# Performance work log

Hardware: AMD Instinct MI355X
Metric: run time of the kernel (lower is better)

Reference implementation:

```python
import jax, jax.numpy as jnp
import numpy as np

N_NODES = 100000
D_IN = 128
D_OUT = 128
B, T, S = 8, 4096, 25


def setup_inputs() -> dict:
    key = jax.random.key(0)
    k1, k2, k3 = jax.random.split(key, 3)
    features = jax.random.normal(k1, (N_NODES, D_IN), dtype=jnp.float32)
    sample_res = jax.random.randint(k2, (B, T, S), 0, N_NODES, dtype=jnp.int64)
    # glorot-uniform init for [D_IN, D_OUT]
    limit = np.sqrt(6.0 / (D_IN + D_OUT)).astype(np.float32)
    weights = jax.random.uniform(k3, (D_IN, D_OUT), dtype=jnp.float32,
                                 minval=-limit, maxval=limit)
    return {"features": features, "sample_res": sample_res, "weights": weights}


def reference(features, sample_res, weights):
    # gather neighbor embeddings: [B, T, S, D]
    sampled = features[sample_res]
    # mean over sampled-neighbor axis -> [B, T, D]
    neigh_vecs = jnp.mean(sampled, axis=2)
    # shared linear transform + relu (bias=False per init defaults)
    out = jnp.einsum('btd,do->bto', neigh_vecs, weights)
    return jax.nn.relu(out)
```

## Files before the change

kernel.cpp:

```cpp
#include <hip/hip_runtime.h>


#define DEG 25
#define DIM 128
#define NPP 25000
#define NPP1 25001

typedef __attribute__((ext_vector_type(8))) short short8;
typedef __attribute__((ext_vector_type(4))) float floatx4;
typedef __attribute__((ext_vector_type(4))) unsigned int uintx4;

__device__ __forceinline__ unsigned short f2bf(float f) {
    unsigned u = __float_as_uint(f);
    return (unsigned short)((u + 0x7fffu + ((u >> 16) & 1u)) >> 16);
}

#define BSTRIDE 136

__global__ __launch_bounds__(256, 2) void gemm_fw(
    const float* __restrict__ A,
    const float* __restrict__ B,
    unsigned short* __restrict__ G,
    int M)
{
    __shared__ unsigned short sBt[DIM * BSTRIDE];

    const int tid = threadIdx.x;

    {
        const float4* B4 = (const float4*)B;
#pragma unroll
        for (int i = 0; i < 16; ++i) {
            const int linear = i * 256 + tid;
            const int k  = linear >> 5;
            const int c4 = linear & 31;
            const float4 v = B4[linear];
            const int n = c4 * 4;
            sBt[(n + 0) * BSTRIDE + k] = f2bf(v.x);
            sBt[(n + 1) * BSTRIDE + k] = f2bf(v.y);
            sBt[(n + 2) * BSTRIDE + k] = f2bf(v.z);
            sBt[(n + 3) * BSTRIDE + k] = f2bf(v.w);
        }
    }
    __syncthreads();

    const int wave = tid >> 6;
    const int lane = tid & 63;
    const int quad = lane >> 4;
    const int l16  = lane & 15;

    const int rw0 = blockIdx.x * 128 + wave * 32;

    floatx4 acc[2][8];
#pragma unroll
    for (int mt = 0; mt < 2; ++mt)
#pragma unroll
        for (int nt = 0; nt < 8; ++nt)
            acc[mt][nt] = (floatx4){0.f, 0.f, 0.f, 0.f};

#pragma unroll
    for (int kt = 0; kt < 4; ++kt) {
        const int k0 = kt * 32;

        short8 afrag[2];
#pragma unroll
        for (int mt = 0; mt < 2; ++mt) {
            int row = rw0 + mt * 16 + l16;
            if (row >= M) row = M - 1;
            const float* ap = A + (size_t)row * DIM + k0 + quad * 8;
            const float4 x = *(const float4*)ap;
            const float4 y = *(const float4*)(ap + 4);
            unsigned p0 = (unsigned)f2bf(x.x) | ((unsigned)f2bf(x.y) << 16);
            unsigned p1 = (unsigned)f2bf(x.z) | ((unsigned)f2bf(x.w) << 16);
            unsigned p2 = (unsigned)f2bf(y.x) | ((unsigned)f2bf(y.y) << 16);
            unsigned p3 = (unsigned)f2bf(y.z) | ((unsigned)f2bf(y.w) << 16);
            uintx4 packed = (uintx4){p0, p1, p2, p3};
            afrag[mt] = __builtin_bit_cast(short8, packed);
        }

#pragma unroll
        for (int nt = 0; nt < 8; ++nt) {
            const uintx4 u = *(const uintx4*)&sBt[(nt * 16 + l16) * BSTRIDE + k0 + quad * 8];
            const short8 bfrag = __builtin_bit_cast(short8, u);
#pragma unroll
            for (int mt = 0; mt < 2; ++mt)
                acc[mt][nt] = __builtin_amdgcn_mfma_f32_16x16x32_bf16(
                    afrag[mt], bfrag, acc[mt][nt], 0, 0, 0);
        }
    }

    __syncthreads();
    {
        unsigned short* sT = sBt + wave * (32 * BSTRIDE);
#pragma unroll
        for (int mt = 0; mt < 2; ++mt)
#pragma unroll
            for (int nt = 0; nt < 8; ++nt)
#pragma unroll
                for (int r = 0; r < 4; ++r)
                    sT[(mt * 16 + quad * 4 + r) * BSTRIDE + nt * 16 + l16] =
                        f2bf(acc[mt][nt][r]);
    }
    __syncthreads();
    {
        const unsigned short* sT = sBt + wave * (32 * BSTRIDE);
        const int oct   = lane & 7;
        const int nrow8 = lane >> 3;
        uintx4* G4 = (uintx4*)G;
#pragma unroll
        for (int g = 0; g < 4; ++g) {
            const int lrow = g * 8 + nrow8;
            const int node = rw0 + lrow;
            if (node < M) {
                const unsigned p     = (unsigned)node / NPP;
                const unsigned local = (unsigned)node - p * NPP;
#pragma unroll
                for (int h = 0; h < 2; ++h) {
                    const uintx4 u = *(const uintx4*)
                        &sT[lrow * BSTRIDE + h * 64 + oct * 8];
                    __builtin_nontemporal_store(u,
                        &G4[((size_t)(p * 2 + h) * NPP1 + local) * 8 + oct]);
                }
            }
        }
        if (blockIdx.x == 0 && tid < 64) {
            const int sl = tid >> 3, o = tid & 7;
            __builtin_nontemporal_store((uintx4){0, 0, 0, 0},
                &G4[((size_t)sl * NPP1 + NPP) * 8 + o]);
        }
    }
}

#define GRB 64

__global__ __launch_bounds__(256, 4) void gather_phased(
    const unsigned short* __restrict__ G,
    const int* __restrict__ idx,
    float* __restrict__ out,
    int n_rows)
{
    __shared__ int sRaw[GRB * DEG];
    __shared__ int sC[GRB][4][25];
    __shared__ int sCnt[GRB][4];

    const int tid  = threadIdx.x;
    const int h    = blockIdx.x & 1;
    const int rb   = blockIdx.x >> 1;
    const int row0 = rb * GRB;

    const int* ib = idx + (size_t)row0 * DEG;
    for (int i = tid; i < GRB * DEG; i += 256)
        sRaw[i] = __builtin_nontemporal_load(ib + i);
    __syncthreads();

    {
        const int row = tid >> 2;
        const int rg  = tid & 3;
        const int lo  = rg * NPP;
        int* dst = &sC[row][rg][0];
        int cnt = 0;
#pragma unroll
        for (int s = 0; s < DEG; ++s) {
            const unsigned d = (unsigned)(sRaw[row * DEG + s] - lo);
            if (d < NPP) dst[cnt++] = (int)d;
        }
        const int m = ((cnt + 4) / 5) * 5;
        for (int i = cnt; i < m; ++i) dst[i] = NPP;
        sCnt[row][rg] = m;
    }
    __syncthreads();

    const int oct   = tid & 7;
    const int rslot = tid >> 3;

    float acc[2][8];
#pragma unroll
    for (int rr = 0; rr < 2; ++rr)
#pragma unroll
        for (int j = 0; j < 8; ++j) acc[rr][j] = 0.f;

    for (int p = 0; p < 4; ++p) {
        const uintx4* __restrict__ Gc =
            (const uintx4*)G + (size_t)(p * 2 + h) * NPP1 * 8 + oct;
#pragma unroll
        for (int rr = 0; rr < 2; ++rr) {
            const int r = rslot + rr * 32;
            const int m = sCnt[r][p];
            const int* lp = &sC[r][p][0];
            for (int i = 0; i < m; i += 5) {
                const uintx4 v0 = Gc[(size_t)lp[i + 0] * 8];
                const uintx4 v1 = Gc[(size_t)lp[i + 1] * 8];
                const uintx4 v2 = Gc[(size_t)lp[i + 2] * 8];
                const uintx4 v3 = Gc[(size_t)lp[i + 3] * 8];
                const uintx4 v4 = Gc[(size_t)lp[i + 4] * 8];
#pragma unroll
                for (int k = 0; k < 5; ++k) {
                    const uintx4 v = (k == 0) ? v0 : (k == 1) ? v1 :
                                     (k == 2) ? v2 : (k == 3) ? v3 : v4;
                    acc[rr][0] += __uint_as_float(v.x << 16);
                    acc[rr][1] += __uint_as_float(v.x & 0xffff0000u);
                    acc[rr][2] += __uint_as_float(v.y << 16);
                    acc[rr][3] += __uint_as_float(v.y & 0xffff0000u);
                    acc[rr][4] += __uint_as_float(v.z << 16);
                    acc[rr][5] += __uint_as_float(v.z & 0xffff0000u);
                    acc[rr][6] += __uint_as_float(v.w << 16);
                    acc[rr][7] += __uint_as_float(v.w & 0xffff0000u);
                }
            }
        }
    }

    const float inv = 1.0f / 25.0f;
#pragma unroll
    for (int rr = 0; rr < 2; ++rr) {
        const int r = rslot + rr * 32;
        floatx4* op = (floatx4*)(out + (size_t)(row0 + r) * DIM + h * 64 + oct * 8);
        const floatx4 o0 = {fmaxf(acc[rr][0] * inv, 0.f), fmaxf(acc[rr][1] * inv, 0.f),
                            fmaxf(acc[rr][2] * inv, 0.f), fmaxf(acc[rr][3] * inv, 0.f)};
        const floatx4 o1 = {fmaxf(acc[rr][4] * inv, 0.f), fmaxf(acc[rr][5] * inv, 0.f),
                            fmaxf(acc[rr][6] * inv, 0.f), fmaxf(acc[rr][7] * inv, 0.f)};
        __builtin_nontemporal_store(o0, op);
        __builtin_nontemporal_store(o1, op + 1);
    }
}

#define RPB 16
#define CG 32

__device__ __forceinline__ float4 relu4(float4 v) {
    return make_float4(fmaxf(v.x, 0.f), fmaxf(v.y, 0.f),
                       fmaxf(v.z, 0.f), fmaxf(v.w, 0.f));
}

__global__ __launch_bounds__(256, 4) void gcn_fused(
    const float* __restrict__ F, const int* __restrict__ idx,
    const float* __restrict__ W, float* __restrict__ out, int n_rows)
{
    __shared__ float4 sV[RPB * CG];
    __shared__ int    sIdx[RPB * DEG];

    const float4* F4 = (const float4*)F;
    const float4* W4 = (const float4*)W;
    float4* out4 = (float4*)out;

    const int tid = threadIdx.x;
    const int row0 = blockIdx.x * RPB;

    for (int i = tid; i < RPB * DEG; i += 256)
        sIdx[i] = idx[(size_t)row0 * DEG + i];
    __syncthreads();

    const int cg = tid & 31;
    const int rs = tid >> 5;

#pragma unroll
    for (int rr = 0; rr < 2; ++rr) {
        const int r = rs + rr * 8;
        int j[DEG];
#pragma unroll
        for (int s = 0; s < DEG; ++s) j[s] = sIdx[r * DEG + s];
        float4 acc = make_float4(0.f, 0.f, 0.f, 0.f);
#pragma unroll
        for (int s = 0; s < DEG; ++s) {
            float4 f = F4[(size_t)j[s] * CG + cg];
            acc.x += f.x; acc.y += f.y; acc.z += f.z; acc.w += f.w;
        }
        const float inv = 1.0f / 25.0f;
        acc.x *= inv; acc.y *= inv; acc.z *= inv; acc.w *= inv;
        sV[r * CG + cg] = acc;
    }
    __syncthreads();

    const float4* vA = &sV[rs * CG];
    const float4* vB = &sV[(rs + 8) * CG];
    float4 o0 = make_float4(0.f, 0.f, 0.f, 0.f);
    float4 o1 = make_float4(0.f, 0.f, 0.f, 0.f);
#pragma unroll 4
    for (int d4 = 0; d4 < CG; ++d4) {
        const float4 a = vA[d4];
        const float4 b = vB[d4];
        const float4 w0 = W4[(size_t)(4 * d4 + 0) * CG + cg];
        const float4 w1 = W4[(size_t)(4 * d4 + 1) * CG + cg];
        const float4 w2 = W4[(size_t)(4 * d4 + 2) * CG + cg];
        const float4 w3 = W4[(size_t)(4 * d4 + 3) * CG + cg];
        o0.x += a.x*w0.x + a.y*w1.x + a.z*w2.x + a.w*w3.x;
        o0.y += a.x*w0.y + a.y*w1.y + a.z*w2.y + a.w*w3.y;
        o0.z += a.x*w0.z + a.y*w1.z + a.z*w2.z + a.w*w3.z;
        o0.w += a.x*w0.w + a.y*w1.w + a.z*w2.w + a.w*w3.w;
        o1.x += b.x*w0.x + b.y*w1.x + b.z*w2.x + b.w*w3.x;
        o1.y += b.x*w0.y + b.y*w1.y + b.z*w2.y + b.w*w3.y;
        o1.z += b.x*w0.z + b.y*w1.z + b.z*w2.z + b.w*w3.z;
        o1.w += b.x*w0.w + b.y*w1.w + b.z*w2.w + b.w*w3.w;
    }
    out4[(size_t)(row0 + rs) * CG + cg]     = relu4(o0);
    out4[(size_t)(row0 + rs + 8) * CG + cg] = relu4(o1);
}

extern "C" void kernel_launch(void* const* d_in, const int* in_sizes, int n_in,
                              void* d_out, int out_size, void* d_ws, size_t ws_size,
                              hipStream_t stream) {
    const float* F   = (const float*)d_in[0];
    const int*   idx = (const int*)d_in[1];
    const float* W   = (const float*)d_in[2];
    float* out = (float*)d_out;

    const int n_nodes = in_sizes[0] / DIM;
    const int n_rows  = in_sizes[1] / DEG;

    const size_t need = (size_t)8 * NPP1 * 64 * sizeof(unsigned short);

    if (n_nodes == 100000 && ws_size >= need && (n_rows & (GRB - 1)) == 0) {
        unsigned short* G = (unsigned short*)d_ws;
        gemm_fw<<<(n_nodes + 127) / 128, 256, 0, stream>>>(F, W, G, n_nodes);
        gather_phased<<<(n_rows / GRB) * 2, 256, 0, stream>>>(G, idx, out, n_rows);
    } else {
        gcn_fused<<<n_rows / RPB, 256, 0, stream>>>(F, idx, W, out, n_rows);
    }
}
```

Before: 128.6 us.

## Halve gather block rows, use ushort index lists, software-pipeline neighbor loads

The phased gather kernel now handles 32 rows per block with one row per 8-thread group instead of two, and targets 6 blocks per SM instead of 4. Compacted neighbor indices are stored as 16-bit values padded to multiples of 4, shrinking shared memory. The inner loop is software-pipelined: the next four bf16 rows are loaded before the current four are accumulated. The aim is more waves in flight and more overlapped memory latency on this random-gather-bound kernel. The cost is more blocks, more redundant index staging, and at least 4 padding loads per partition even when it has no neighbors.

```diff
diff --git a/kernel.cpp b/kernel.cpp
--- a/kernel.cpp
+++ b/kernel.cpp
@@ -131,16 +131,16 @@
     }
 }
 
-#define GRB 64
-
-__global__ __launch_bounds__(256, 4) void gather_phased(
+#define GRB 32
+
+__global__ __launch_bounds__(256, 6) void gather_phased(
     const unsigned short* __restrict__ G,
     const int* __restrict__ idx,
     float* __restrict__ out,
     int n_rows)
 {
     __shared__ int sRaw[GRB * DEG];
-    __shared__ int sC[GRB][4][25];
+    __shared__ unsigned short sC[GRB][4][28];
     __shared__ int sCnt[GRB][4];
 
     const int tid  = threadIdx.x;
@@ -153,75 +153,72 @@
         sRaw[i] = __builtin_nontemporal_load(ib + i);
     __syncthreads();
 
-    {
+    if (tid < GRB * 4) {
         const int row = tid >> 2;
         const int rg  = tid & 3;
         const int lo  = rg * NPP;
-        int* dst = &sC[row][rg][0];
+        unsigned short* dst = &sC[row][rg][0];
         int cnt = 0;
 #pragma unroll
         for (int s = 0; s < DEG; ++s) {
             const unsigned d = (unsigned)(sRaw[row * DEG + s] - lo);
-            if (d < NPP) dst[cnt++] = (int)d;
-        }
-        const int m = ((cnt + 4) / 5) * 5;
-        for (int i = cnt; i < m; ++i) dst[i] = NPP;
+            if (d < NPP) dst[cnt++] = (unsigned short)d;
+        }
+        int m = ((cnt + 3) / 4) * 4;
+        if (m == 0) m = 4;
+        for (int i = cnt; i < m; ++i) dst[i] = (unsigned short)NPP;
         sCnt[row][rg] = m;
     }
     __syncthreads();
 
-    const int oct   = tid & 7;
-    const int rslot = tid >> 3;
-
-    float acc[2][8];
-#pragma unroll
-    for (int rr = 0; rr < 2; ++rr)
-#pragma unroll
-        for (int j = 0; j < 8; ++j) acc[rr][j] = 0.f;
+    const int oct = tid & 7;
+    const int r   = tid >> 3;
+
+    float a0 = 0.f, a1 = 0.f, a2 = 0.f, a3 = 0.f;
+    float a4 = 0.f, a5 = 0.f, a6 = 0.f, a7 = 0.f;
+
+#define ACC8(v)                                 \
+    do {                                        \
+        a0 += __uint_as_float((v).x << 16);     \
+        a1 += __uint_as_float((v).x & 0xffff0000u); \
+        a2 += __uint_as_float((v).y << 16);     \
+        a3 += __uint_as_float((v).y & 0xffff0000u); \
+        a4 += __uint_as_float((v).z << 16);     \
+        a5 += __uint_as_float((v).z & 0xffff0000u); \
+        a6 += __uint_as_float((v).w << 16);     \
+        a7 += __uint_as_float((v).w & 0xffff0000u); \
+    } while (0)
 
     for (int p = 0; p < 4; ++p) {
         const uintx4* __restrict__ Gc =
             (const uintx4*)G + (size_t)(p * 2 + h) * NPP1 * 8 + oct;
-#pragma unroll
-        for (int rr = 0; rr < 2; ++rr) {
-            const int r = rslot + rr * 32;
-            const int m = sCnt[r][p];
-            const int* lp = &sC[r][p][0];
-            for (int i = 0; i < m; i += 5) {
-                const uintx4 v0 = Gc[(size_t)lp[i + 0] * 8];
-                const uintx4 v1 = Gc[(size_t)lp[i + 1] * 8];
-                const uintx4 v2 = Gc[(size_t)lp[i + 2] * 8];
-                const uintx4 v3 = Gc[(size_t)lp[i + 3] * 8];
-                const uintx4 v4 = Gc[(size_t)lp[i + 4] * 8];
-#pragma unroll
-                for (int k = 0; k < 5; ++k) {
-                    const uintx4 v = (k == 0) ? v0 : (k == 1) ? v1 :
-                                     (k == 2) ? v2 : (k == 3) ? v3 : v4;
-                    acc[rr][0] += __uint_as_float(v.x << 16);
-                    acc[rr][1] += __uint_as_float(v.x & 0xffff0000u);
-                    acc[rr][2] += __uint_as_float(v.y << 16);
-                    acc[rr][3] += __uint_as_float(v.y & 0xffff0000u);
-                    acc[rr][4] += __uint_as_float(v.z << 16);
-                    acc[rr][5] += __uint_as_float(v.z & 0xffff0000u);
-                    acc[rr][6] += __uint_as_float(v.w << 16);
-                    acc[rr][7] += __uint_as_float(v.w & 0xffff0000u);
-                }
-            }
-        }
-    }
+        const unsigned short* lp = &sC[r][p][0];
+        const int m = sCnt[r][p];
+
+        uintx4 v0 = Gc[(size_t)lp[0] * 8];
+        uintx4 v1 = Gc[(size_t)lp[1] * 8];
+        uintx4 v2 = Gc[(size_t)lp[2] * 8];
+        uintx4 v3 = Gc[(size_t)lp[3] * 8];
+        for (int i = 4; i < m; i += 4) {
+            const uintx4 w0 = Gc[(size_t)lp[i + 0] * 8];
+            const uintx4 w1 = Gc[(size_t)lp[i + 1] * 8];
+            const uintx4 w2 = Gc[(size_t)lp[i + 2] * 8];
+            const uintx4 w3 = Gc[(size_t)lp[i + 3] * 8];
+            ACC8(v0); ACC8(v1); ACC8(v2); ACC8(v3);
+            v0 = w0; v1 = w1; v2 = w2; v3 = w3;
+        }
+        ACC8(v0); ACC8(v1); ACC8(v2); ACC8(v3);
+    }
+#undef ACC8
 
     const float inv = 1.0f / 25.0f;
-#pragma unroll
-    for (int rr = 0; rr < 2; ++rr) {
-        const int r = rslot + rr * 32;
-        floatx4* op = (floatx4*)(out + (size_t)(row0 + r) * DIM + h * 64 + oct * 8);
-        const floatx4 o0 = {fmaxf(acc[rr][0] * inv, 0.f), fmaxf(acc[rr][1] * inv, 0.f),
-                            fmaxf(acc[rr][2] * inv, 0.f), fmaxf(acc[rr][3] * inv, 0.f)};
-        const floatx4 o1 = {fmaxf(acc[rr][4] * inv, 0.f), fmaxf(acc[rr][5] * inv, 0.f),
-                            fmaxf(acc[rr][6] * inv, 0.f), fmaxf(acc[rr][7] * inv, 0.f)};
-        __builtin_nontemporal_store(o0, op);
-        __builtin_nontemporal_store(o1, op + 1);
-    }
+    floatx4* op = (floatx4*)(out + (size_t)(row0 + r) * DIM + h * 64 + oct * 8);
+    const floatx4 o0 = {fmaxf(a0 * inv, 0.f), fmaxf(a1 * inv, 0.f),
+                        fmaxf(a2 * inv, 0.f), fmaxf(a3 * inv, 0.f)};
+    const floatx4 o1 = {fmaxf(a4 * inv, 0.f), fmaxf(a5 * inv, 0.f),
+                        fmaxf(a6 * inv, 0.f), fmaxf(a7 * inv, 0.f)};
+    __builtin_nontemporal_store(o0, op);
+    __builtin_nontemporal_store(o1, op + 1);
 }
 
 #define RPB 16
```

Measured after the change: 129.5 us. About the same (+0.7%).
